# Performance work log

Hardware: AMD Instinct MI355X
Metric: run time of the kernel (lower is better)

## Reference

```python
import jax, jax.numpy as jnp
import numpy as np

N_QUBITS = 4
N_LAYERS = 2
BN_EPS = 1e-5


def _bcast(t, ref):
    t = jnp.asarray(t)
    return t.reshape(t.shape + (1,) * (ref.ndim - t.ndim))


def apply_ry(state, theta, wire):
    # state: [B, 2,2,2,2] complex; theta: scalar or [B]
    ax = wire + 1
    s0 = jnp.take(state, 0, axis=ax)
    s1 = jnp.take(state, 1, axis=ax)
    half = jnp.asarray(theta, jnp.float32) * 0.5
    c = _bcast(jnp.cos(half), s0)
    s = _bcast(jnp.sin(half), s0)
    return jnp.stack([c * s0 - s * s1, s * s0 + c * s1], axis=ax)


def apply_rz(state, theta, wire):
    ax = wire + 1
    s0 = jnp.take(state, 0, axis=ax)
    s1 = jnp.take(state, 1, axis=ax)
    half = jnp.asarray(theta, jnp.float32) * 0.5
    p = _bcast(jnp.exp(-1j * half), s0)  # complex64
    return jnp.stack([p * s0, jnp.conj(p) * s1], axis=ax)


def apply_cnot(state, control, target):
    ca, ta = control + 1, target + 1
    c0 = jnp.take(state, 0, axis=ca)
    c1 = jnp.take(state, 1, axis=ca)
    ta2 = ta - 1 if ta > ca else ta  # axis shift after take
    c1 = jnp.flip(c1, axis=ta2)      # X on target within control=1 block
    return jnp.stack([c0, c1], axis=ca)


def quantum_layer(x_q_in, qw):
    # Faithful to QuantumLayer.forward: extra tanh on (already tanh'd) input.
    B = x_q_in.shape[0]
    ang = jnp.tanh(x_q_in) * jnp.float32(np.pi)  # [B, n_qubits]
    state = jnp.zeros((B, 2 ** N_QUBITS), jnp.complex64).at[:, 0].set(1.0)
    state = state.reshape((B,) + (2,) * N_QUBITS)
    for i in range(N_QUBITS):
        state = apply_ry(state, ang[:, i], i)
    for l in range(N_LAYERS):
        for i in range(N_QUBITS):
            state = apply_ry(state, qw[l, i, 0], i)
            state = apply_rz(state, qw[l, i, 1], i)
        for i in range(N_QUBITS):
            state = apply_cnot(state, i, (i + 1) % N_QUBITS)
    probs = state.real ** 2 + state.imag ** 2  # [B,2,2,2,2]
    zs = []
    for i in range(N_QUBITS):
        d = jnp.take(probs, 0, axis=i + 1) - jnp.take(probs, 1, axis=i + 1)
        zs.append(jnp.sum(d, axis=tuple(range(1, d.ndim))))
    return jnp.stack(zs, axis=1).astype(jnp.float32)  # [B, n_qubits]


def forward(x, W1, b1, bn_g, bn_b, bn_m, bn_v, W2, b2, qw, W3, b3):
    # pre_quantum (eval mode: dropouts are identity)
    h = jax.nn.relu(x @ W1.T + b1)                       # [B,64]
    h = (h - bn_m) * jax.lax.rsqrt(bn_v + BN_EPS) * bn_g + bn_b
    xq = jnp.tanh(h @ W2.T + b2)                          # [B,4]
    q = quantum_layer(xq, qw)                             # [B,4]
    return q @ W3.T + b3                                  # [B,num_classes]


def setup_inputs() -> dict:
    key = jax.random.key(0)
    ks = jax.random.split(key, 8)
    B, D, H, Q, C = 32768, 1280, 64, N_QUBITS, 10
    return {
        "x": jax.random.normal(ks[0], (B, D), jnp.float32),
        "W1": jax.random.normal(ks[1], (H, D), jnp.float32) * 0.02,
        "b1": jnp.zeros((H,), jnp.float32),
        "bn_g": jnp.ones((H,), jnp.float32),
        "bn_b": jnp.zeros((H,), jnp.float32),
        "bn_m": jnp.zeros((H,), jnp.float32),
        "bn_v": jnp.ones((H,), jnp.float32),
        "W2": jax.random.normal(ks[2], (Q, H), jnp.float32) * 0.1,
        "b2": jnp.zeros((Q,), jnp.float32),
        "qw": jax.random.normal(ks[3], (N_LAYERS, Q, 2), jnp.float32) * 0.1,
        "W3": jax.random.normal(ks[4], (C, Q), jnp.float32) * 0.1,
        "b3": jnp.zeros((C,), jnp.float32),
    }


def reference(x, W1, b1, bn_g, bn_b, bn_m, bn_v, W2, b2, qw, W3, b3):
    return forward(x, W1, b1, bn_g, bn_b, bn_m, bn_v, W2, b2, qw, W3, b3)
```

## Files before the change

kernel.cpp:

```cpp
#include <hip/hip_runtime.h>
#include <math.h>

typedef __attribute__((ext_vector_type(8))) short bf16x8;
typedef __attribute__((ext_vector_type(4))) float f32x4;

constexpr int D   = 1280;
constexpr int H   = 64;
constexpr int BM  = 128;
constexpr int NT  = 512;
constexpr int KC  = 64;
constexpr int SW  = KC + 8;
constexpr int HSS = H + 1;

union FragU { bf16x8 v; unsigned int u[4]; };

__device__ __forceinline__ unsigned int pack_split(float f0, float f1, unsigned int& lo) {
    unsigned int u0 = __float_as_uint(f0), u1 = __float_as_uint(f1);
    unsigned int h0 = u0 & 0xFFFF0000u,    h1 = u1 & 0xFFFF0000u;
    float l0 = f0 - __uint_as_float(h0);
    float l1 = f1 - __uint_as_float(h1);
    lo = (__float_as_uint(l1) & 0xFFFF0000u) | (__float_as_uint(l0) >> 16);
    return h1 | (u0 >> 16);
}

template<int BW>
__device__ __forceinline__ void ry_gate(float re[16], float im[16], float theta) {
    float sn, cs;
    sincosf(0.5f * theta, &sn, &cs);
#pragma unroll
    for (int s0 = 0; s0 < 16; ++s0) {
        if (s0 & BW) continue;
        const int s1 = s0 | BW;
        float r0 = re[s0], i0 = im[s0], r1 = re[s1], i1 = im[s1];
        re[s0] = cs * r0 - sn * r1;  im[s0] = cs * i0 - sn * i1;
        re[s1] = sn * r0 + cs * r1;  im[s1] = sn * i0 + cs * i1;
    }
}

template<int BW>
__device__ __forceinline__ void rz_gate(float re[16], float im[16], float theta) {
    float sn, cs;
    sincosf(0.5f * theta, &sn, &cs);
#pragma unroll
    for (int s0 = 0; s0 < 16; ++s0) {
        if (s0 & BW) continue;
        const int s1 = s0 | BW;
        float r0 = re[s0], i0 = im[s0], r1 = re[s1], i1 = im[s1];
        re[s0] = cs * r0 + sn * i0;  im[s0] = cs * i0 - sn * r0;
        re[s1] = cs * r1 - sn * i1;  im[s1] = cs * i1 + sn * r1;
    }
}

template<int BWC, int BWT>
__device__ __forceinline__ void cnot_gate(float re[16], float im[16]) {
#pragma unroll
    for (int s = 0; s < 16; ++s) {
        if (!(s & BWC)) continue;
        if (s & BWT) continue;
        const int t = s | BWT;
        float tr = re[s], ti = im[s];
        re[s] = re[t]; im[s] = im[t];
        re[t] = tr;    im[t] = ti;
    }
}

__device__ __forceinline__ void quantum_row(const float ang[4], const float* __restrict__ qw,
                                            const float* __restrict__ W3, const float* __restrict__ b3,
                                            float* __restrict__ o) {
    float re[16] = {}, im[16] = {};
    re[0] = 1.0f;
    ry_gate<8>(re, im, ang[0]);
    ry_gate<4>(re, im, ang[1]);
    ry_gate<2>(re, im, ang[2]);
    ry_gate<1>(re, im, ang[3]);
#pragma unroll
    for (int ll = 0; ll < 2; ++ll) {
        const float* qp = &qw[ll * 8];
        ry_gate<8>(re, im, qp[0]); rz_gate<8>(re, im, qp[1]);
        ry_gate<4>(re, im, qp[2]); rz_gate<4>(re, im, qp[3]);
        ry_gate<2>(re, im, qp[4]); rz_gate<2>(re, im, qp[5]);
        ry_gate<1>(re, im, qp[6]); rz_gate<1>(re, im, qp[7]);
        cnot_gate<8, 4>(re, im);
        cnot_gate<4, 2>(re, im);
        cnot_gate<2, 1>(re, im);
        cnot_gate<1, 8>(re, im);
    }
    float z[4] = {};
#pragma unroll
    for (int s = 0; s < 16; ++s) {
        float p = re[s] * re[s] + im[s] * im[s];
        z[0] += (s & 8) ? -p : p;
        z[1] += (s & 4) ? -p : p;
        z[2] += (s & 2) ? -p : p;
        z[3] += (s & 1) ? -p : p;
    }
#pragma unroll
    for (int c = 0; c < 10; ++c) {
        float v = b3[c];
#pragma unroll
        for (int i = 0; i < 4; ++i)
            v = fmaf(z[i], W3[c * 4 + i], v);
        o[c] = v;
    }
}

__global__ __launch_bounds__(512, 2)
void fused_qh_v9(const float* __restrict__ x,   const float* __restrict__ W1,
                 const float* __restrict__ b1,  const float* __restrict__ bn_g,
                 const float* __restrict__ bn_b,const float* __restrict__ bn_m,
                 const float* __restrict__ bn_v,const float* __restrict__ W2,
                 const float* __restrict__ b2,  const float* __restrict__ qw,
                 const float* __restrict__ W3,  const float* __restrict__ b3,
                 float* __restrict__ out)
{
    __shared__ short whi[H][SW];
    __shared__ short wlo[H][SW];
    __shared__ float hs[BM][HSS];
    __shared__ float w2s[4 * H];
    __shared__ float b1s[H], scl[H], shf[H];
    __shared__ float angs[BM][4];

    const int tid  = threadIdx.x;
    const int l    = tid & 63;
    const int w    = tid >> 6;
    const int lr   = l & 15;
    const int lk   = l >> 4;
    const int row0 = blockIdx.x * BM;

    if (tid < 256) w2s[tid] = W2[tid];
    if (tid < H) {
        float s = bn_g[tid] * rsqrtf(bn_v[tid] + 1e-5f);
        b1s[tid] = b1[tid];
        scl[tid] = s;
        shf[tid] = bn_b[tid] - bn_m[tid] * s;
    }

    const float4* xr4 = reinterpret_cast<const float4*>(x + (size_t)(row0 + w * 16 + lr) * D);

    int sn[2], sk4[2];
#pragma unroll
    for (int it = 0; it < 2; ++it) {
        int f4 = tid + it * 512;
        sn[it]  = f4 >> 4;
        sk4[it] = (f4 & 15) * 4;
    }

    f32x4 acc[4] = {{0,0,0,0},{0,0,0,0},{0,0,0,0},{0,0,0,0}};
    float4 acur[4], anxt[4], wcur[2], wnxt[2];
#pragma unroll
    for (int it = 0; it < 2; ++it)
        wcur[it] = *reinterpret_cast<const float4*>(&W1[(size_t)sn[it] * D + sk4[it]]);
#pragma unroll
    for (int h = 0; h < 2; ++h)
#pragma unroll
        for (int p = 0; p < 2; ++p)
            acur[h * 2 + p] = xr4[h * 8 + lk * 2 + p];

    for (int k0 = 0; k0 < D; k0 += KC) {
#pragma unroll
        for (int it = 0; it < 2; ++it) {
            unsigned int lo01, lo23;
            unsigned int hi01 = pack_split(wcur[it].x, wcur[it].y, lo01);
            unsigned int hi23 = pack_split(wcur[it].z, wcur[it].w, lo23);
            uint2 hv; hv.x = hi01; hv.y = hi23;
            uint2 lv; lv.x = lo01; lv.y = lo23;
            *reinterpret_cast<uint2*>(&whi[sn[it]][sk4[it]]) = hv;
            *reinterpret_cast<uint2*>(&wlo[sn[it]][sk4[it]]) = lv;
        }
        if (k0 + KC < D) {
            const int kn = k0 + KC;
#pragma unroll
            for (int it = 0; it < 2; ++it)
                wnxt[it] = *reinterpret_cast<const float4*>(&W1[(size_t)sn[it] * D + kn + sk4[it]]);
#pragma unroll
            for (int h = 0; h < 2; ++h)
#pragma unroll
                for (int p = 0; p < 2; ++p)
                    anxt[h * 2 + p] = xr4[kn / 4 + h * 8 + lk * 2 + p];
        }
        __syncthreads();

        FragU ahi[2], alo[2];
#pragma unroll
        for (int h = 0; h < 2; ++h) {
            const float4 p0 = acur[h * 2 + 0];
            const float4 p1 = acur[h * 2 + 1];
            ahi[h].u[0] = pack_split(p0.x, p0.y, alo[h].u[0]);
            ahi[h].u[1] = pack_split(p0.z, p0.w, alo[h].u[1]);
            ahi[h].u[2] = pack_split(p1.x, p1.y, alo[h].u[2]);
            ahi[h].u[3] = pack_split(p1.z, p1.w, alo[h].u[3]);
        }

#pragma unroll
        for (int h = 0; h < 2; ++h)
#pragma unroll
            for (int g = 0; g < 4; ++g) {
                const bf16x8 bh = *reinterpret_cast<const bf16x8*>(&whi[g * 16 + lr][h * 32 + lk * 8]);
                const bf16x8 bl = *reinterpret_cast<const bf16x8*>(&wlo[g * 16 + lr][h * 32 + lk * 8]);
                acc[g] = __builtin_amdgcn_mfma_f32_16x16x32_bf16(ahi[h].v, bh, acc[g], 0, 0, 0);
                acc[g] = __builtin_amdgcn_mfma_f32_16x16x32_bf16(ahi[h].v, bl, acc[g], 0, 0, 0);
                acc[g] = __builtin_amdgcn_mfma_f32_16x16x32_bf16(alo[h].v, bh, acc[g], 0, 0, 0);
            }
        __syncthreads();

#pragma unroll
        for (int it = 0; it < 2; ++it) wcur[it] = wnxt[it];
#pragma unroll
        for (int i = 0; i < 4; ++i) acur[i] = anxt[i];
    }

#pragma unroll
    for (int g = 0; g < 4; ++g) {
        const int cc = g * 16 + lr;
        const float b1c = b1s[cc], s = scl[cc], sh = shf[cc];
#pragma unroll
        for (int r = 0; r < 4; ++r) {
            float v = acc[g][r] + b1c;
            v = fmaxf(v, 0.0f) * s + sh;
            hs[w * 16 + lk * 4 + r][cc] = v;
        }
    }
    __syncthreads();

    {
        const int row = tid >> 2, qi = tid & 3;
        float a2v = b2[qi];
#pragma unroll
        for (int k = 0; k < H; ++k)
            a2v = fmaf(hs[row][k], w2s[qi * H + k], a2v);
        float xq = tanhf(a2v);
        angs[row][qi] = tanhf(xq) * 3.14159265358979323846f;
    }
    __syncthreads();

    if (tid < BM) {
        float ang[4] = { angs[tid][0], angs[tid][1], angs[tid][2], angs[tid][3] };
        quantum_row(ang, qw, W3, b3, &out[(size_t)(row0 + tid) * 10]);
    }
}

extern "C" void kernel_launch(void* const* d_in, const int* in_sizes, int n_in,
                              void* d_out, int out_size, void* d_ws, size_t ws_size,
                              hipStream_t stream) {
    const float* x    = (const float*)d_in[0];
    const float* W1   = (const float*)d_in[1];
    const float* b1   = (const float*)d_in[2];
    const float* bn_g = (const float*)d_in[3];
    const float* bn_b = (const float*)d_in[4];
    const float* bn_m = (const float*)d_in[5];
    const float* bn_v = (const float*)d_in[6];
    const float* W2   = (const float*)d_in[7];
    const float* b2   = (const float*)d_in[8];
    const float* qw   = (const float*)d_in[9];
    const float* W3   = (const float*)d_in[10];
    const float* b3   = (const float*)d_in[11];
    float* out = (float*)d_out;

    const int B = in_sizes[0] / D;
    const int grid = B / BM;

    fused_qh_v9<<<grid, NT, 0, stream>>>(
        x, W1, b1, bn_g, bn_b, bn_m, bn_v, W2, b2, qw, W3, b3, out);
}
```

Before: 43.48 us.

## Split GEMM1 over K halves into two kernels with workspace reduction

Replaces the single fused kernel with a split-K GEMM kernel that uses 64-row tiles and two K halves, writing partial sums to a workspace. A second kernel then sums the partials and runs the BN, the second linear layer and the quantum circuit. The aim is more blocks and better occupancy for the memory-bound x read. The cost is 16 MB of extra workspace traffic and a second launch. It only takes this path when the workspace is large enough and B matches the hardcoded row count.

```diff
diff --git a/kernel.cpp b/kernel.cpp
--- a/kernel.cpp
+++ b/kernel.cpp
@@ -6,11 +6,11 @@
 
 constexpr int D   = 1280;
 constexpr int H   = 64;
-constexpr int BM  = 128;
-constexpr int NT  = 512;
 constexpr int KC  = 64;
 constexpr int SW  = KC + 8;
 constexpr int HSS = H + 1;
+constexpr int KHALF = D / 2;
+constexpr int ROWS_TOTAL = 32768;
 
 union FragU { bf16x8 v; unsigned int u[4]; };
 
@@ -103,6 +103,171 @@
         o[c] = v;
     }
 }
+
+__global__ __launch_bounds__(256, 4)
+void gemm1_partial(const float* __restrict__ x, const float* __restrict__ W1,
+                   float* __restrict__ pws)
+{
+    __shared__ short whi[H][SW];
+    __shared__ short wlo[H][SW];
+
+    const int tid  = threadIdx.x;
+    const int l    = tid & 63;
+    const int w    = tid >> 6;
+    const int lr   = l & 15;
+    const int lk   = l >> 4;
+    const int kh   = blockIdx.x & 1;
+    const int row0 = (blockIdx.x >> 1) * 64;
+    const int kbase = kh * KHALF;
+
+    const float4* xr4 = reinterpret_cast<const float4*>(x + (size_t)(row0 + w * 16 + lr) * D);
+
+    int sn[4], sk4[4];
+#pragma unroll
+    for (int it = 0; it < 4; ++it) {
+        int f4 = tid + it * 256;
+        sn[it]  = f4 >> 4;
+        sk4[it] = (f4 & 15) * 4;
+    }
+
+    f32x4 acc[4] = {{0,0,0,0},{0,0,0,0},{0,0,0,0},{0,0,0,0}};
+    float4 acur[4], anxt[4], wcur[4], wnxt[4];
+#pragma unroll
+    for (int it = 0; it < 4; ++it)
+        wcur[it] = *reinterpret_cast<const float4*>(&W1[(size_t)sn[it] * D + kbase + sk4[it]]);
+#pragma unroll
+    for (int h = 0; h < 2; ++h)
+#pragma unroll
+        for (int p = 0; p < 2; ++p)
+            acur[h * 2 + p] = xr4[kbase / 4 + h * 8 + lk * 2 + p];
+
+    for (int k0 = kbase; k0 < kbase + KHALF; k0 += KC) {
+#pragma unroll
+        for (int it = 0; it < 4; ++it) {
+            unsigned int lo01, lo23;
+            unsigned int hi01 = pack_split(wcur[it].x, wcur[it].y, lo01);
+            unsigned int hi23 = pack_split(wcur[it].z, wcur[it].w, lo23);
+            uint2 hv; hv.x = hi01; hv.y = hi23;
+            uint2 lv; lv.x = lo01; lv.y = lo23;
+            *reinterpret_cast<uint2*>(&whi[sn[it]][sk4[it]]) = hv;
+            *reinterpret_cast<uint2*>(&wlo[sn[it]][sk4[it]]) = lv;
+        }
+        if (k0 + KC < kbase + KHALF) {
+            const int kn = k0 + KC;
+#pragma unroll
+            for (int it = 0; it < 4; ++it)
+                wnxt[it] = *reinterpret_cast<const float4*>(&W1[(size_t)sn[it] * D + kn + sk4[it]]);
+#pragma unroll
+            for (int h = 0; h < 2; ++h)
+#pragma unroll
+                for (int p = 0; p < 2; ++p)
+                    anxt[h * 2 + p] = xr4[kn / 4 + h * 8 + lk * 2 + p];
+        }
+        __syncthreads();
+
+        FragU ahi[2], alo[2];
+#pragma unroll
+        for (int h = 0; h < 2; ++h) {
+            const float4 p0 = acur[h * 2 + 0];
+            const float4 p1 = acur[h * 2 + 1];
+            ahi[h].u[0] = pack_split(p0.x, p0.y, alo[h].u[0]);
+            ahi[h].u[1] = pack_split(p0.z, p0.w, alo[h].u[1]);
+            ahi[h].u[2] = pack_split(p1.x, p1.y, alo[h].u[2]);
+            ahi[h].u[3] = pack_split(p1.z, p1.w, alo[h].u[3]);
+        }
+#pragma unroll
+        for (int h = 0; h < 2; ++h)
+#pragma unroll
+            for (int g = 0; g < 4; ++g) {
+                const bf16x8 bh = *reinterpret_cast<const bf16x8*>(&whi[g * 16 + lr][h * 32 + lk * 8]);
+                const bf16x8 bl = *reinterpret_cast<const bf16x8*>(&wlo[g * 16 + lr][h * 32 + lk * 8]);
+                acc[g] = __builtin_amdgcn_mfma_f32_16x16x32_bf16(ahi[h].v, bh, acc[g], 0, 0, 0);
+                acc[g] = __builtin_amdgcn_mfma_f32_16x16x32_bf16(ahi[h].v, bl, acc[g], 0, 0, 0);
+                acc[g] = __builtin_amdgcn_mfma_f32_16x16x32_bf16(alo[h].v, bh, acc[g], 0, 0, 0);
+            }
+        __syncthreads();
+
+#pragma unroll
+        for (int it = 0; it < 4; ++it) { acur[it] = anxt[it]; wcur[it] = wnxt[it]; }
+    }
+
+    float* base = pws + (size_t)kh * ROWS_TOTAL * H;
+#pragma unroll
+    for (int g = 0; g < 4; ++g) {
+        const int cc = g * 16 + lr;
+#pragma unroll
+        for (int r = 0; r < 4; ++r) {
+            const int row = row0 + w * 16 + lk * 4 + r;
+            base[(size_t)row * H + cc] = acc[g][r];
+        }
+    }
+}
+
+__global__ __launch_bounds__(256, 4)
+void finish_qh(const float* __restrict__ pws,
+               const float* __restrict__ b1,  const float* __restrict__ bn_g,
+               const float* __restrict__ bn_b,const float* __restrict__ bn_m,
+               const float* __restrict__ bn_v,const float* __restrict__ W2,
+               const float* __restrict__ b2,  const float* __restrict__ qw,
+               const float* __restrict__ W3,  const float* __restrict__ b3,
+               float* __restrict__ out)
+{
+    __shared__ float hs[64][HSS];
+    __shared__ float w2s[4 * H];
+    __shared__ float b1s[H], scl[H], shf[H];
+    __shared__ float angs[64][4];
+
+    const int tid  = threadIdx.x;
+    const int row0 = blockIdx.x * 64;
+
+    w2s[tid] = W2[tid];
+    if (tid < H) {
+        float s = bn_g[tid] * rsqrtf(bn_v[tid] + 1e-5f);
+        b1s[tid] = b1[tid];
+        scl[tid] = s;
+        shf[tid] = bn_b[tid] - bn_m[tid] * s;
+    }
+    __syncthreads();
+
+    {
+        const int r  = tid >> 2;
+        const int cb = (tid & 3) * 16;
+        const float4* p0 = reinterpret_cast<const float4*>(pws + (size_t)(row0 + r) * H + cb);
+        const float4* p1 = reinterpret_cast<const float4*>(pws + (size_t)ROWS_TOTAL * H + (size_t)(row0 + r) * H + cb);
+#pragma unroll
+        for (int j = 0; j < 4; ++j) {
+            const float4 a = p0[j];
+            const float4 b = p1[j];
+            float vv[4] = { a.x + b.x, a.y + b.y, a.z + b.z, a.w + b.w };
+#pragma unroll
+            for (int q = 0; q < 4; ++q) {
+                const int c = cb + j * 4 + q;
+                float v = vv[q] + b1s[c];
+                v = fmaxf(v, 0.0f) * scl[c] + shf[c];
+                hs[r][c] = v;
+            }
+        }
+    }
+    __syncthreads();
+
+    {
+        const int row = tid >> 2, qi = tid & 3;
+        float a2v = b2[qi];
+#pragma unroll
+        for (int k = 0; k < H; ++k)
+            a2v = fmaf(hs[row][k], w2s[qi * H + k], a2v);
+        float xq = tanhf(a2v);
+        angs[row][qi] = tanhf(xq) * 3.14159265358979323846f;
+    }
+    __syncthreads();
+
+    if (tid < 64) {
+        float ang[4] = { angs[tid][0], angs[tid][1], angs[tid][2], angs[tid][3] };
+        quantum_row(ang, qw, W3, b3, &out[(size_t)(row0 + tid) * 10]);
+    }
+}
+
+constexpr int BM9 = 128;
 
 __global__ __launch_bounds__(512, 2)
 void fused_qh_v9(const float* __restrict__ x,   const float* __restrict__ W1,
@@ -115,17 +280,17 @@
 {
     __shared__ short whi[H][SW];
     __shared__ short wlo[H][SW];
-    __shared__ float hs[BM][HSS];
+    __shared__ float hs[BM9][HSS];
     __shared__ float w2s[4 * H];
     __shared__ float b1s[H], scl[H], shf[H];
-    __shared__ float angs[BM][4];
+    __shared__ float angs[BM9][4];
 
     const int tid  = threadIdx.x;
     const int l    = tid & 63;
     const int w    = tid >> 6;
     const int lr   = l & 15;
     const int lk   = l >> 4;
-    const int row0 = blockIdx.x * BM;
+    const int row0 = blockIdx.x * BM9;
 
     if (tid < 256) w2s[tid] = W2[tid];
     if (tid < H) {
@@ -190,7 +355,6 @@
             ahi[h].u[2] = pack_split(p1.x, p1.y, alo[h].u[2]);
             ahi[h].u[3] = pack_split(p1.z, p1.w, alo[h].u[3]);
         }
-
 #pragma unroll
         for (int h = 0; h < 2; ++h)
 #pragma unroll
@@ -233,7 +397,7 @@
     }
     __syncthreads();
 
-    if (tid < BM) {
+    if (tid < BM9) {
         float ang[4] = { angs[tid][0], angs[tid][1], angs[tid][2], angs[tid][3] };
         quantum_row(ang, qw, W3, b3, &out[(size_t)(row0 + tid) * 10]);
     }
@@ -257,8 +421,15 @@
     float* out = (float*)d_out;
 
     const int B = in_sizes[0] / D;
-    const int grid = B / BM;
-
-    fused_qh_v9<<<grid, NT, 0, stream>>>(
-        x, W1, b1, bn_g, bn_b, bn_m, bn_v, W2, b2, qw, W3, b3, out);
-}
+
+    const size_t need = (size_t)2 * ROWS_TOTAL * H * sizeof(float);
+    if (ws_size >= need && B == ROWS_TOTAL) {
+        float* pws = (float*)d_ws;
+        gemm1_partial<<<(B / 64) * 2, 256, 0, stream>>>(x, W1, pws);
+        finish_qh<<<B / 64, 256, 0, stream>>>(
+            pws, b1, bn_g, bn_b, bn_m, bn_v, W2, b2, qw, W3, b3, out);
+    } else {
+        fused_qh_v9<<<B / BM9, 512, 0, stream>>>(
+            x, W1, b1, bn_g, bn_b, bn_m, bn_v, W2, b2, qw, W3, b3, out);
+    }
+}
```

After: 49.46 us. 1.14x slower.
